# Optimization experiments

Hardware: AMD Instinct MI355X
Metric: run time of the kernel (lower is better)

## Reference

```python
import jax, jax.numpy as jnp
import numpy as np
import math

H = 128            # hidden_size
NBAND = 512        # n_band
NOISE_LEN = 65536  # min_noise_len (power of 2)
SYNTH_WINDOW = 32
FRAME_LEN = NOISE_LEN // SYNTH_WINDOW  # 2048 amplitude frames per synth chunk
B = 2
T = 2048           # control frames; divisible by FRAME_LEN -> 1 chunk
NCP = 2            # n_control_params


def _ln(x, g, b, eps=1e-5):
    m = x.mean(-1, keepdims=True)
    v = ((x - m) ** 2).mean(-1, keepdims=True)
    return (x - m) / jnp.sqrt(v + eps) * g + b


def _mlp_layer(x, W, b, g, beta):
    # Linear -> LayerNorm -> LeakyReLU(0.01), as in mlp()
    y = _ln(x @ W.T + b, g, beta)
    return jnp.where(y >= 0, y, 0.01 * y)


def _gru(x, W_ih, W_hh, b_ih, b_hh):
    # PyTorch GRU, batch_first. x: [B, T, In] -> [B, T, H]
    Hd = W_hh.shape[1]
    xp = x @ W_ih.T + b_ih  # precompute input projections [B, T, 3H]
    def step(h, xt):
        gh = h @ W_hh.T + b_hh
        i_r, i_z, i_n = jnp.split(xt, 3, -1)
        h_r, h_z, h_n = jnp.split(gh, 3, -1)
        r = jax.nn.sigmoid(i_r + h_r)
        z = jax.nn.sigmoid(i_z + h_z)
        n = jnp.tanh(i_n + r * h_n)
        h = (1.0 - z) * n + z * h
        return h, h
    h0 = jnp.zeros((x.shape[0], Hd), x.dtype)
    _, hs = jax.lax.scan(step, h0, jnp.swapaxes(xp, 0, 1))
    return jnp.swapaxes(hs, 0, 1)


def _synth(amplitudes, noise_bands):
    # amplitudes: [B, C, T]; noise_bands: [C, NOISE_LEN]
    # Faithful to synth_batch: per-chunk (frame_len) linear upsample by
    # synth_window (align_corners=False), multiply by noise bands, sum bands.
    Bc, C, Tt = amplitudes.shape
    n_chunks = Tt // FRAME_LEN
    a = amplitudes.reshape(Bc, C, n_chunks, FRAME_LEN)
    j = jnp.arange(NOISE_LEN)
    src = jnp.maximum((j + 0.5) / SYNTH_WINDOW - 0.5, 0.0)
    idx0 = jnp.floor(src).astype(jnp.int32)
    w = (src - idx0).astype(amplitudes.dtype)
    idx1 = jnp.minimum(idx0 + 1, FRAME_LEN - 1)
    # [B, C, n_chunks, NOISE_LEN] upsampled amplitudes
    up = a[..., idx0] * (1.0 - w) + a[..., idx1] * w
    sig = jnp.einsum('bcns,cs->bns', up, noise_bands)
    return sig.reshape(Bc, 1, n_chunks * NOISE_LEN)


def setup_inputs():
    key = jax.random.key(0)
    ks = jax.random.split(key, 16)
    def nrm(k, shape, scale=0.05):
        return jax.random.normal(k, shape, dtype=jnp.float32) * scale
    inp = {}
    inp['cp0'] = jax.random.uniform(ks[0], (B, T, 1), dtype=jnp.float32)
    inp['cp1'] = jax.random.uniform(ks[1], (B, T, 1), dtype=jnp.float32)
    inp['in0_W'] = nrm(ks[2], (H, 1)); inp['in0_b'] = jnp.zeros((H,))
    inp['in0_g'] = jnp.ones((H,)); inp['in0_beta'] = jnp.zeros((H,))
    inp['in1_W'] = nrm(ks[3], (H, 1)); inp['in1_b'] = jnp.zeros((H,))
    inp['in1_g'] = jnp.ones((H,)); inp['in1_beta'] = jnp.zeros((H,))
    inp['gru_Wih'] = nrm(ks[4], (3 * H, NCP * H))
    inp['gru_Whh'] = nrm(ks[5], (3 * H, H))
    inp['gru_bih'] = jnp.zeros((3 * H,)); inp['gru_bhh'] = jnp.zeros((3 * H,))
    dims = [H + NCP, H, H]
    for i in range(3):
        inp['o%d_W' % i] = nrm(ks[6 + i], (H, dims[i]))
        inp['o%d_b' % i] = jnp.zeros((H,))
        inp['o%d_g' % i] = jnp.ones((H,)); inp['o%d_beta' % i] = jnp.zeros((H,))
    inp['amp_W'] = nrm(ks[9], (NBAND, H)); inp['amp_b'] = jnp.zeros((NBAND,))
    # Precomputed noise bands buffer (stands in for the filterbank-derived
    # constant; random roll shift fixed to 0 for determinism).
    inp['noise_bands'] = nrm(ks[10], (NBAND, NOISE_LEN), 1.0)
    return inp


def reference(cp0, cp1, in0_W, in0_b, in0_g, in0_beta, in1_W, in1_b, in1_g, in1_beta,
              gru_Wih, gru_Whh, gru_bih, gru_bhh,
              o0_W, o0_b, o0_g, o0_beta, o1_W, o1_b, o1_g, o1_beta,
              o2_W, o2_b, o2_g, o2_beta, amp_W, amp_b, noise_bands):
    h0 = _mlp_layer(cp0, in0_W, in0_b, in0_g, in0_beta)
    h1 = _mlp_layer(cp1, in1_W, in1_b, in1_g, in1_beta)
    hidden = jnp.concatenate([h0, h1], -1)            # [B, T, 2H]
    hidden = _gru(hidden, gru_Wih, gru_Whh, gru_bih, gru_bhh)  # [B, T, H]
    hidden = jnp.concatenate([hidden, cp0, cp1], -1)  # [B, T, H+2]
    hidden = _mlp_layer(hidden, o0_W, o0_b, o0_g, o0_beta)
    hidden = _mlp_layer(hidden, o1_W, o1_b, o1_g, o1_beta)
    hidden = _mlp_layer(hidden, o2_W, o2_b, o2_g, o2_beta)
    amps = hidden @ amp_W.T + amp_b                   # [B, T, NBAND]
    amps = jnp.transpose(amps, (0, 2, 1))             # [B, NBAND, T]
    amps = 2.0 * jax.nn.sigmoid(amps) ** math.log(10) + 1e-18  # scale_function
    return _synth(amps, noise_bands)                  # [B, 1, T*SYNTH_WINDOW]
```

## Files before the change

### kernel.cpp

```cpp
#include <hip/hip_runtime.h>
#include <hip/hip_bf16.h>
#include <math.h>

#define HDIM 128
#define T3   384
#define NT   2048
#define NBND 512
#define NLEN 65536

__device__ __forceinline__ float sigmoidf_(float x){ return 1.f/(1.f+__expf(-x)); }
__device__ __forceinline__ float tanhf_(float x){ float e=__expf(2.f*x); return 1.f - 2.f/(e+1.f); }

__device__ __forceinline__ float dpp_xor1_(float x){
  int r = __builtin_amdgcn_update_dpp(0, __float_as_int(x), 0xB1, 0xF, 0xF, true);
  return __int_as_float(r);
}
__device__ __forceinline__ float dpp_xor2_(float x){
  int r = __builtin_amdgcn_update_dpp(0, __float_as_int(x), 0x4E, 0xF, 0xF, true);
  return __int_as_float(r);
}
__device__ __forceinline__ float swz_xor4_(float x){
  return __int_as_float(__builtin_amdgcn_ds_swizzle(__float_as_int(x), 0x101F));
}
__device__ __forceinline__ float swz_xor8_(float x){
  return __int_as_float(__builtin_amdgcn_ds_swizzle(__float_as_int(x), 0x201F));
}
__device__ __forceinline__ void pkfma_(float2& acc, float2 a, float2 b){
  asm("v_pk_fma_f32 %0, %1, %2, %0" : "+v"(acc) : "v"(a), "v"(b));
}

__global__ __launch_bounds__(128) void k_inmlp(
    const float* __restrict__ cp0, const float* __restrict__ cp1,
    const float* __restrict__ W0, const float* __restrict__ b0,
    const float* __restrict__ g0, const float* __restrict__ be0,
    const float* __restrict__ W1, const float* __restrict__ b1,
    const float* __restrict__ g1, const float* __restrict__ be1,
    float* __restrict__ hcat)
{
  int bt = blockIdx.x; int i = threadIdx.x;
  float c0 = cp0[bt], c1 = cp1[bt];
  float v0 = fmaf(c0, W0[i], b0[i]);
  float v1 = fmaf(c1, W1[i], b1[i]);
  __shared__ float red[4];
  float s0 = v0, s1 = v1;
  #pragma unroll
  for (int m=1;m<64;m<<=1){ s0 += __shfl_xor(s0,m); s1 += __shfl_xor(s1,m); }
  if ((i&63)==0){ red[(i>>6)*2+0]=s0; red[(i>>6)*2+1]=s1; }
  __syncthreads();
  float m0 = (red[0]+red[2])*(1.f/128.f);
  float m1 = (red[1]+red[3])*(1.f/128.f);
  __syncthreads();
  float d0 = v0-m0, d1 = v1-m1;
  float q0 = d0*d0, q1 = d1*d1;
  #pragma unroll
  for (int m=1;m<64;m<<=1){ q0 += __shfl_xor(q0,m); q1 += __shfl_xor(q1,m); }
  if ((i&63)==0){ red[(i>>6)*2+0]=q0; red[(i>>6)*2+1]=q1; }
  __syncthreads();
  float va0 = (red[0]+red[2])*(1.f/128.f);
  float va1 = (red[1]+red[3])*(1.f/128.f);
  float y0 = d0*rsqrtf(va0+1e-5f)*g0[i] + be0[i];
  float y1 = d1*rsqrtf(va1+1e-5f)*g1[i] + be1[i];
  y0 = y0>=0.f ? y0 : 0.01f*y0;
  y1 = y1>=0.f ? y1 : 0.01f*y1;
  hcat[(size_t)bt*256 + i]       = y0;
  hcat[(size_t)bt*256 + 128 + i] = y1;
}

__global__ __launch_bounds__(256) void k_xp(
    const float* __restrict__ hcat, const float* __restrict__ Wih,
    const float* __restrict__ bih, float* __restrict__ xp)
{
  __shared__ float ht[32][260];
  __shared__ float wTg[96][260];
  int mb = blockIdx.x, nbt = blockIdx.y;
  int tid = threadIdx.x;
  int row0 = mb*32, g0 = nbt*96;
  for (int idx = tid; idx < 32*64; idx += 256){
    int t = idx >> 6, q = idx & 63;
    ((float4*)&ht[t][0])[q] = ((const float4*)(hcat + (size_t)(row0+t)*256))[q];
  }
  for (int idx = tid; idx < 96*64; idx += 256){
    int g = idx >> 6, q = idx & 63;
    ((float4*)&wTg[g][0])[q] = ((const float4*)(Wih + (size_t)(g0+g)*256))[q];
  }
  __syncthreads();
  int tt = tid & 7, gg = tid >> 3;
  float a[4][3] = {};
  for (int k=0;k<256;k+=4){
    float4 hv[4], wv[3];
    hv[0] = *(const float4*)&ht[tt][k];
    hv[1] = *(const float4*)&ht[tt+8][k];
    hv[2] = *(const float4*)&ht[tt+16][k];
    hv[3] = *(const float4*)&ht[tt+24][k];
    wv[0] = *(const float4*)&wTg[gg*3+0][k];
    wv[1] = *(const float4*)&wTg[gg*3+1][k];
    wv[2] = *(const float4*)&wTg[gg*3+2][k];
    #pragma unroll
    for (int ti=0;ti<4;ti++){
      #pragma unroll
      for (int gi=0;gi<3;gi++){
        a[ti][gi] = fmaf(hv[ti].x, wv[gi].x, a[ti][gi]);
        a[ti][gi] = fmaf(hv[ti].y, wv[gi].y, a[ti][gi]);
        a[ti][gi] = fmaf(hv[ti].z, wv[gi].z, a[ti][gi]);
        a[ti][gi] = fmaf(hv[ti].w, wv[gi].w, a[ti][gi]);
      }
    }
  }
  #pragma unroll
  for (int ti=0;ti<4;ti++){
    int row = row0 + tt + 8*ti;
    #pragma unroll
    for (int gi=0;gi<3;gi++){
      int g = g0 + gg*3 + gi;
      xp[(size_t)row*T3 + g] = a[ti][gi] + bih[g];
    }
  }
}

__global__ __launch_bounds__(512, 2) void k_gru(
    const float* __restrict__ xp, const float* __restrict__ Whh,
    const float* __restrict__ bhh, float* __restrict__ hout)
{
  __shared__ float hbuf[2][128];
  int b = blockIdx.x;
  int tid = threadIdx.x;
  int g  = tid >> 3;
  int kh = tid & 7;
  float2 w[6][8];
  #pragma unroll
  for (int i=0;i<6;i++){
    const float2* wr = (const float2*)(Whh + (size_t)(g + (i<<6))*HDIM + (kh<<4));
    #pragma unroll
    for (int c=0;c<8;c++) w[i][c] = wr[c];
  }
  int hr = g + ((kh&1)<<6);
  float br = bhh[hr], bz = bhh[HDIM+hr], bn = bhh[2*HDIM+hr];
  if (tid < 128) hbuf[0][tid] = 0.f;
  const float* xq = xp + (size_t)b*NT*T3;
  float* hob = hout + (size_t)b*NT*HDIM + hr;
  float ir = xq[hr], iz = xq[HDIM+hr], ixn = xq[2*HDIM+hr];
  float hprev = 0.f;
  __syncthreads();
  int cur = 0;
  for (int t=0;t<NT;t++){
    float irn=0.f, izn=0.f, ixnn=0.f;
    if (t+1 < NT){
      const float* xn = xq + (size_t)(t+1)*T3;
      irn = xn[hr]; izn = xn[HDIM+hr]; ixnn = xn[2*HDIM+hr];
    }
    const float2* h2 = (const float2*)(&hbuf[cur][kh<<4]);
    float2 a0={0.f,0.f},a1=a0,a2=a0,a3=a0,a4=a0,a5=a0;
    #pragma unroll
    for (int c=0;c<8;c++){
      float2 hv = h2[c];
      pkfma_(a0, w[0][c], hv);
      pkfma_(a1, w[1][c], hv);
      pkfma_(a2, w[2][c], hv);
      pkfma_(a3, w[3][c], hv);
      pkfma_(a4, w[4][c], hv);
      pkfma_(a5, w[5][c], hv);
    }
    float s0=a0.x+a0.y, s1=a1.x+a1.y, s2=a2.x+a2.y,
          s3=a3.x+a3.y, s4=a4.x+a4.y, s5=a5.x+a5.y;
    s0 += dpp_xor1_(s0); s1 += dpp_xor1_(s1); s2 += dpp_xor1_(s2);
    s3 += dpp_xor1_(s3); s4 += dpp_xor1_(s4); s5 += dpp_xor1_(s5);
    s0 += dpp_xor2_(s0); s1 += dpp_xor2_(s1); s2 += dpp_xor2_(s2);
    s3 += dpp_xor2_(s3); s4 += dpp_xor2_(s4); s5 += dpp_xor2_(s5);
    bool odd = (kh & 1);
    float u0 = odd ? s1 : s0;
    float u1 = odd ? s3 : s2;
    float u2 = odd ? s5 : s4;
    float T0 = u0 + swz_xor4_(u0);
    float T1 = u1 + swz_xor4_(u1);
    float T2 = u2 + swz_xor4_(u2);
    float rr = sigmoidf_(ir + T0 + br);
    float zz = sigmoidf_(iz + T1 + bz);
    float nn = tanhf_(fmaf(rr, T2 + bn, ixn));
    float hn = fmaf(zz, hprev - nn, nn);
    if (kh < 2){
      hbuf[cur^1][hr] = hn;
      hob[(size_t)t*HDIM] = hn;
      hprev = hn;
    }
    __syncthreads();
    cur ^= 1;
    ir = irn; iz = izn; ixn = ixnn;
  }
}

__global__ __launch_bounds__(256, 2) void k_post(
    const float* __restrict__ hout, const float* __restrict__ cp0, const float* __restrict__ cp1,
    const float* __restrict__ o0W, const float* __restrict__ o0b, const float* __restrict__ o0g, const float* __restrict__ o0be,
    const float* __restrict__ o1W, const float* __restrict__ o1b, const float* __restrict__ o1g, const float* __restrict__ o1be,
    const float* __restrict__ o2W, const float* __restrict__ o2b, const float* __restrict__ o2g, const float* __restrict__ o2be,
    const float* __restrict__ ampW, const float* __restrict__ ampb,
    float* __restrict__ amps)
{
  __shared__ float A[16][136];
  __shared__ float Bf[16][136];
  __shared__ float lng[128], lnb[128];
  int blk = blockIdx.x;
  int b = blk >> 7, tc = blk & 127;
  int bt0 = b*NT + tc*16;
  int tid = threadIdx.x;
  int kh = tid & 1, o = tid >> 1;
  for (int idx = tid; idx < 16*32; idx += 256){
    int t = idx >> 5, q = idx & 31;
    ((float4*)&A[t][0])[q] = ((const float4*)(hout + (size_t)(bt0+t)*HDIM))[q];
  }
  if (tid < 16){
    int bt = bt0 + tid;
    A[tid][128] = cp0[bt]; A[tid][129] = cp1[bt];
    #pragma unroll
    for (int z=130; z<136; z++){ A[tid][z] = 0.f; Bf[tid][z] = 0.f; }
    Bf[tid][128] = 0.f; Bf[tid][129] = 0.f;
  }
  __syncthreads();
  const float* Ws[3] = {o0W, o1W, o2W};
  const float* Bs[3] = {o0b, o1b, o2b};
  const float* Gs[3] = {o0g, o1g, o2g};
  const float* Es[3] = {o0be, o1be, o2be};
  const int kds[3] = {130, 128, 128};
  float (*src)[136] = A;
  float (*dst)[136] = Bf;
  for (int l=0; l<3; l++){
    const int kd = kds[l];
    const float* W = Ws[l];
    if (tid < 128){ lng[tid] = Gs[l][tid]; lnb[tid] = Es[l][tid]; }
    float w[68];
    #pragma unroll
    for (int c=0;c<68;c++){
      int k = kh*68 + c;
      w[c] = (k < kd) ? W[(size_t)o*kd + k] : 0.f;
    }
    float bias = (kh==0) ? Bs[l][o] : 0.f;
    float acc16[16];
    #pragma unroll
    for (int t=0;t<16;t++){
      float acc = bias;
      const float* ar = &src[t][kh*68];
      #pragma unroll
      for (int c=0;c<68;c++) acc = fmaf(w[c], ar[c], acc);
      acc16[t] = acc;
    }
    #pragma unroll
    for (int t=0;t<16;t++) acc16[t] += dpp_xor1_(acc16[t]);
    if (kh==0){
      #pragma unroll
      for (int t=0;t<16;t++) dst[t][o] = acc16[t];
    }
    __syncthreads();
    {
      int t = tid >> 4, j = tid & 15;
      float4 v0 = ((float4*)&dst[t][0])[j*2];
      float4 v1 = ((float4*)&dst[t][0])[j*2+1];
      float sm = v0.x+v0.y+v0.z+v0.w + v1.x+v1.y+v1.z+v1.w;
      float sq = v0.x*v0.x+v0.y*v0.y+v0.z*v0.z+v0.w*v0.w
               + v1.x*v1.x+v1.y*v1.y+v1.z*v1.z+v1.w*v1.w;
      sm += dpp_xor1_(sm); sq += dpp_xor1_(sq);
      sm += dpp_xor2_(sm); sq += dpp_xor2_(sq);
      sm += swz_xor4_(sm); sq += swz_xor4_(sq);
      sm += swz_xor8_(sm); sq += swz_xor8_(sq);
      float mean = sm * (1.f/128.f);
      float var  = sq * (1.f/128.f) - mean*mean;
      float rs = rsqrtf(var + 1e-5f);
      float o8[8] = {v0.x,v0.y,v0.z,v0.w,v1.x,v1.y,v1.z,v1.w};
      #pragma unroll
      for (int e=0;e<8;e++){
        int oc = j*8+e;
        float y = (o8[e]-mean)*rs*lng[oc] + lnb[oc];
        o8[e] = y>=0.f ? y : 0.01f*y;
      }
      ((float4*)&dst[t][0])[j*2]   = make_float4(o8[0],o8[1],o8[2],o8[3]);
      ((float4*)&dst[t][0])[j*2+1] = make_float4(o8[4],o8[5],o8[6],o8[7]);
    }
    __syncthreads();
    { float (*tmp)[136] = src; src = dst; dst = tmp; }
  }
  #pragma unroll 1
  for (int ch=0; ch<4; ch++){
    int oc = ch*128 + o;
    float w[68];
    #pragma unroll
    for (int c=0;c<68;c++){
      int k = kh*68 + c;
      w[c] = (k < 128) ? ampW[(size_t)oc*HDIM + k] : 0.f;
    }
    float bias = (kh==0) ? ampb[oc] : 0.f;
    #pragma unroll
    for (int t=0;t<16;t++){
      float acc = bias;
      const float* ar = &src[t][kh*68];
      #pragma unroll
      for (int c=0;c<68;c++) acc = fmaf(w[c], ar[c], acc);
      acc += dpp_xor1_(acc);
      if (kh==0){
        float sg = sigmoidf_(acc);
        float p = __powf(sg, 2.3025850929940457f);
        amps[(size_t)(bt0+t)*NBND + oc] = 2.f*p + 1e-18f;
      }
    }
  }
}

__global__ __launch_bounds__(256) void k_synth(
    const float* __restrict__ amps, const float* __restrict__ nbands,
    float* __restrict__ out)
{
  __shared__ float SA[2*10*516];
  int blk = blockIdx.x;
  int tid = threadIdx.x;
  int s = blk*256 + tid;
  int tbase = blk*8 - 1; if (tbase < 0) tbase = 0;
  for (int idx = tid; idx < 2*10*128; idx += 256){
    int bb  = idx / 1280;
    int rem = idx - bb*1280;
    int ttl = rem >> 7;
    int q   = rem & 127;
    int tg = tbase + ttl; if (tg > NT-1) tg = NT-1;
    ((float4*)&SA[bb*5160 + ttl*516])[q] =
        ((const float4*)(amps + (size_t)(bb*NT + tg)*NBND))[q];
  }
  __syncthreads();
  float srcp = fmaxf((s + 0.5f)*(1.f/32.f) - 0.5f, 0.f);
  int i0 = (int)srcp;
  float w = srcp - (float)i0;
  int i1 = i0 + 1; if (i1 > NT-1) i1 = NT-1;
  int l0 = i0 - tbase, l1 = i1 - tbase;
  const float4* A0 = (const float4*)(SA + l0*516);
  const float4* A1 = (const float4*)(SA + l1*516);
  const float4* B0 = (const float4*)(SA + 5160 + l0*516);
  const float4* B1 = (const float4*)(SA + 5160 + l1*516);
  float acc0 = 0.f, acc1 = 0.f;
  const float* nb = nbands + s;
  for (int c4=0;c4<128;c4++){
    float4 a0v = A0[c4], a1v = A1[c4], b0v = B0[c4], b1v = B1[c4];
    size_t cb = (size_t)(c4*4)*NLEN;
    float n0 = nb[cb], n1 = nb[cb+(size_t)NLEN], n2 = nb[cb+2*(size_t)NLEN], n3 = nb[cb+3*(size_t)NLEN];
    acc0 = fmaf(fmaf(w, a1v.x - a0v.x, a0v.x), n0, acc0);
    acc0 = fmaf(fmaf(w, a1v.y - a0v.y, a0v.y), n1, acc0);
    acc0 = fmaf(fmaf(w, a1v.z - a0v.z, a0v.z), n2, acc0);
    acc0 = fmaf(fmaf(w, a1v.w - a0v.w, a0v.w), n3, acc0);
    acc1 = fmaf(fmaf(w, b1v.x - b0v.x, b0v.x), n0, acc1);
    acc1 = fmaf(fmaf(w, b1v.y - b0v.y, b0v.y), n1, acc1);
    acc1 = fmaf(fmaf(w, b1v.z - b0v.z, b0v.z), n2, acc1);
    acc1 = fmaf(fmaf(w, b1v.w - b0v.w, b0v.w), n3, acc1);
  }
  out[s]        = acc0;
  out[NLEN + s] = acc1;
}

extern "C" void kernel_launch(void* const* d_in, const int* in_sizes, int n_in,
                              void* d_out, int out_size, void* d_ws, size_t ws_size,
                              hipStream_t stream)
{
  const float* cp0   = (const float*)d_in[0];
  const float* cp1   = (const float*)d_in[1];
  const float* in0W  = (const float*)d_in[2];
  const float* in0b  = (const float*)d_in[3];
  const float* in0g  = (const float*)d_in[4];
  const float* in0be = (const float*)d_in[5];
  const float* in1W  = (const float*)d_in[6];
  const float* in1b  = (const float*)d_in[7];
  const float* in1g  = (const float*)d_in[8];
  const float* in1be = (const float*)d_in[9];
  const float* Wih   = (const float*)d_in[10];
  const float* Whh   = (const float*)d_in[11];
  const float* bih   = (const float*)d_in[12];
  const float* bhh   = (const float*)d_in[13];
  const float* o0W = (const float*)d_in[14]; const float* o0b = (const float*)d_in[15];
  const float* o0g = (const float*)d_in[16]; const float* o0be = (const float*)d_in[17];
  const float* o1W = (const float*)d_in[18]; const float* o1b = (const float*)d_in[19];
  const float* o1g = (const float*)d_in[20]; const float* o1be = (const float*)d_in[21];
  const float* o2W = (const float*)d_in[22]; const float* o2b = (const float*)d_in[23];
  const float* o2g = (const float*)d_in[24]; const float* o2be = (const float*)d_in[25];
  const float* ampW = (const float*)d_in[26];
  const float* ampb = (const float*)d_in[27];
  const float* nbnd = (const float*)d_in[28];

  float* ws   = (float*)d_ws;
  float* hcat = ws;
  float* xp   = hcat + 4096*256;
  float* hout = xp   + 4096*384;
  float* amps = hout + 4096*128;

  k_inmlp<<<dim3(4096), dim3(128), 0, stream>>>(cp0, cp1, in0W, in0b, in0g, in0be,
                                                in1W, in1b, in1g, in1be, hcat);
  k_xp<<<dim3(128,4), dim3(256), 0, stream>>>(hcat, Wih, bih, xp);
  k_gru<<<dim3(2), dim3(512), 0, stream>>>(xp, Whh, bhh, hout);
  k_post<<<dim3(256), dim3(256), 0, stream>>>(hout, cp0, cp1,
                                              o0W, o0b, o0g, o0be,
                                              o1W, o1b, o1g, o1be,
                                              o2W, o2b, o2g, o2be,
                                              ampW, ampb, amps);
  k_synth<<<dim3(256), dim3(256), 0, stream>>>(amps, nbnd, (float*)d_out);
}
```

Before: 2.179 ms.

## Tighten GRU step reduction and LDS layout; halve post-MLP tile for more blocks

In the GRU, the hidden-state buffer is padded per 16-element slice and read with float4 loads. The cross-lane reduction replaces the select plus ds_swizzle with a third DPP add, which shortens the serial per-timestep latency. The launch-bounds occupancy hint is dropped and hprev is now updated in every lane. The post-MLP kernel processes 8 timesteps per block instead of 16, doubling the grid, and splits each dot product over two accumulators to shorten FMA chains, at the cost of reloading weights per block.

Measured after the change: 1.759 ms. -19.3%, faster.

```diff
diff --git a/kernel.cpp b/kernel.cpp
--- a/kernel.cpp
+++ b/kernel.cpp
@@ -17,6 +17,10 @@
 }
 __device__ __forceinline__ float dpp_xor2_(float x){
   int r = __builtin_amdgcn_update_dpp(0, __float_as_int(x), 0x4E, 0xF, 0xF, true);
+  return __int_as_float(r);
+}
+__device__ __forceinline__ float dpp_xor7_(float x){
+  int r = __builtin_amdgcn_update_dpp(0, __float_as_int(x), 0x141, 0xF, 0xF, true);
   return __int_as_float(r);
 }
 __device__ __forceinline__ float swz_xor4_(float x){
@@ -117,11 +121,11 @@
   }
 }
 
-__global__ __launch_bounds__(512, 2) void k_gru(
+__global__ __launch_bounds__(512) void k_gru(
     const float* __restrict__ xp, const float* __restrict__ Whh,
     const float* __restrict__ bhh, float* __restrict__ hout)
 {
-  __shared__ float hbuf[2][128];
+  __shared__ float hbuf[2][8][20];
   int b = blockIdx.x;
   int tid = threadIdx.x;
   int g  = tid >> 3;
@@ -133,9 +137,10 @@
     #pragma unroll
     for (int c=0;c<8;c++) w[i][c] = wr[c];
   }
-  int hr = g + ((kh&1)<<6);
+  int par = kh & 1;
+  int hr = g + (par<<6);
   float br = bhh[hr], bz = bhh[HDIM+hr], bn = bhh[2*HDIM+hr];
-  if (tid < 128) hbuf[0][tid] = 0.f;
+  if (tid < 128) hbuf[0][tid>>4][tid&15] = 0.f;
   const float* xq = xp + (size_t)b*NT*T3;
   float* hob = hout + (size_t)b*NT*HDIM + hr;
   float ir = xq[hr], iz = xq[HDIM+hr], ixn = xq[2*HDIM+hr];
@@ -148,7 +153,13 @@
       const float* xn = xq + (size_t)(t+1)*T3;
       irn = xn[hr]; izn = xn[HDIM+hr]; ixnn = xn[2*HDIM+hr];
     }
-    const float2* h2 = (const float2*)(&hbuf[cur][kh<<4]);
+    const float4* hsl = (const float4*)&hbuf[cur][kh][0];
+    float4 hv0 = hsl[0], hv1 = hsl[1], hv2 = hsl[2], hv3 = hsl[3];
+    float2 h2[8];
+    h2[0] = make_float2(hv0.x, hv0.y); h2[1] = make_float2(hv0.z, hv0.w);
+    h2[2] = make_float2(hv1.x, hv1.y); h2[3] = make_float2(hv1.z, hv1.w);
+    h2[4] = make_float2(hv2.x, hv2.y); h2[5] = make_float2(hv2.z, hv2.w);
+    h2[6] = make_float2(hv3.x, hv3.y); h2[7] = make_float2(hv3.z, hv3.w);
     float2 a0={0.f,0.f},a1=a0,a2=a0,a3=a0,a4=a0,a5=a0;
     #pragma unroll
     for (int c=0;c<8;c++){
@@ -166,21 +177,19 @@
     s3 += dpp_xor1_(s3); s4 += dpp_xor1_(s4); s5 += dpp_xor1_(s5);
     s0 += dpp_xor2_(s0); s1 += dpp_xor2_(s1); s2 += dpp_xor2_(s2);
     s3 += dpp_xor2_(s3); s4 += dpp_xor2_(s4); s5 += dpp_xor2_(s5);
-    bool odd = (kh & 1);
-    float u0 = odd ? s1 : s0;
-    float u1 = odd ? s3 : s2;
-    float u2 = odd ? s5 : s4;
-    float T0 = u0 + swz_xor4_(u0);
-    float T1 = u1 + swz_xor4_(u1);
-    float T2 = u2 + swz_xor4_(u2);
+    s0 += dpp_xor7_(s0); s1 += dpp_xor7_(s1); s2 += dpp_xor7_(s2);
+    s3 += dpp_xor7_(s3); s4 += dpp_xor7_(s4); s5 += dpp_xor7_(s5);
+    float T0 = par ? s1 : s0;
+    float T1 = par ? s3 : s2;
+    float T2 = par ? s5 : s4;
     float rr = sigmoidf_(ir + T0 + br);
     float zz = sigmoidf_(iz + T1 + bz);
     float nn = tanhf_(fmaf(rr, T2 + bn, ixn));
     float hn = fmaf(zz, hprev - nn, nn);
+    hprev = hn;
     if (kh < 2){
-      hbuf[cur^1][hr] = hn;
+      hbuf[cur^1][hr>>4][hr&15] = hn;
       hob[(size_t)t*HDIM] = hn;
-      hprev = hn;
     }
     __syncthreads();
     cur ^= 1;
@@ -196,19 +205,19 @@
     const float* __restrict__ ampW, const float* __restrict__ ampb,
     float* __restrict__ amps)
 {
-  __shared__ float A[16][136];
-  __shared__ float Bf[16][136];
+  __shared__ float A[8][136];
+  __shared__ float Bf[8][136];
   __shared__ float lng[128], lnb[128];
   int blk = blockIdx.x;
-  int b = blk >> 7, tc = blk & 127;
-  int bt0 = b*NT + tc*16;
+  int b = blk >> 8, tc = blk & 255;
+  int bt0 = b*NT + tc*8;
   int tid = threadIdx.x;
   int kh = tid & 1, o = tid >> 1;
-  for (int idx = tid; idx < 16*32; idx += 256){
-    int t = idx >> 5, q = idx & 31;
+  {
+    int t = tid >> 5, q = tid & 31;
     ((float4*)&A[t][0])[q] = ((const float4*)(hout + (size_t)(bt0+t)*HDIM))[q];
   }
-  if (tid < 16){
+  if (tid < 8){
     int bt = bt0 + tid;
     A[tid][128] = cp0[bt]; A[tid][129] = cp1[bt];
     #pragma unroll
@@ -234,23 +243,29 @@
       w[c] = (k < kd) ? W[(size_t)o*kd + k] : 0.f;
     }
     float bias = (kh==0) ? Bs[l][o] : 0.f;
-    float acc16[16];
-    #pragma unroll
-    for (int t=0;t<16;t++){
-      float acc = bias;
-      const float* ar = &src[t][kh*68];
+    float acc8[8];
+    #pragma unroll
+    for (int t=0;t<8;t++){
+      const float4* ar4 = (const float4*)&src[t][kh*68];
+      float acc = bias, acc2 = 0.f;
       #pragma unroll
-      for (int c=0;c<68;c++) acc = fmaf(w[c], ar[c], acc);
-      acc16[t] = acc;
-    }
-    #pragma unroll
-    for (int t=0;t<16;t++) acc16[t] += dpp_xor1_(acc16[t]);
+      for (int c4=0;c4<17;c4++){
+        float4 av = ar4[c4];
+        acc  = fmaf(w[c4*4+0], av.x, acc);
+        acc2 = fmaf(w[c4*4+1], av.y, acc2);
+        acc  = fmaf(w[c4*4+2], av.z, acc);
+        acc2 = fmaf(w[c4*4+3], av.w, acc2);
+      }
+      acc8[t] = acc + acc2;
+    }
+    #pragma unroll
+    for (int t=0;t<8;t++) acc8[t] += dpp_xor1_(acc8[t]);
     if (kh==0){
       #pragma unroll
-      for (int t=0;t<16;t++) dst[t][o] = acc16[t];
+      for (int t=0;t<8;t++) dst[t][o] = acc8[t];
     }
     __syncthreads();
-    {
+    if (tid < 128){
       int t = tid >> 4, j = tid & 15;
       float4 v0 = ((float4*)&dst[t][0])[j*2];
       float4 v1 = ((float4*)&dst[t][0])[j*2+1];
@@ -288,11 +303,18 @@
     }
     float bias = (kh==0) ? ampb[oc] : 0.f;
     #pragma unroll
-    for (int t=0;t<16;t++){
-      float acc = bias;
-      const float* ar = &src[t][kh*68];
+    for (int t=0;t<8;t++){
+      const float4* ar4 = (const float4*)&src[t][kh*68];
+      float acc = bias, acc2 = 0.f;
       #pragma unroll
-      for (int c=0;c<68;c++) acc = fmaf(w[c], ar[c], acc);
+      for (int c4=0;c4<17;c4++){
+        float4 av = ar4[c4];
+        acc  = fmaf(w[c4*4+0], av.x, acc);
+        acc2 = fmaf(w[c4*4+1], av.y, acc2);
+        acc  = fmaf(w[c4*4+2], av.z, acc);
+        acc2 = fmaf(w[c4*4+3], av.w, acc2);
+      }
+      acc = acc + acc2;
       acc += dpp_xor1_(acc);
       if (kh==0){
         float sg = sigmoidf_(acc);
@@ -388,7 +410,7 @@
                                                 in1W, in1b, in1g, in1be, hcat);
   k_xp<<<dim3(128,4), dim3(256), 0, stream>>>(hcat, Wih, bih, xp);
   k_gru<<<dim3(2), dim3(512), 0, stream>>>(xp, Whh, bhh, hout);
-  k_post<<<dim3(256), dim3(256), 0, stream>>>(hout, cp0, cp1,
+  k_post<<<dim3(512), dim3(256), 0, stream>>>(hout, cp0, cp1,
                                               o0W, o0b, o0g, o0be,
                                               o1W, o1b, o1g, o1be,
                                               o2W, o2b, o2g, o2be,
```
